# Kernel tuning notes

Measured on AMD Instinct MI355X. Metric: run time of the kernel, lower is better.

## Reference

```python
import jax, jax.numpy as jnp
import numpy as np

V, E, LD, NLANG, H, B, T = 8000, 150, 50, 10, 512, 100, 50
D0 = E + LD  # layer-0 GRU input size


def setup_inputs() -> dict:
    key = jax.random.key(0)
    ks = jax.random.split(key, 12)
    iw = 0.5 / E  # TF init_width
    def rn(k, shape, s=0.05):
        return jax.random.normal(k, shape, jnp.float32) * s
    return {
        "input_data": jax.random.randint(ks[0], (B, T), 0, V, jnp.int32),
        "langs": jax.random.randint(ks[1], (B,), 0, NLANG, jnp.int32),
        "targets": jax.random.randint(ks[2], (B, T), 0, V, jnp.int32),
        "embedding": jax.random.uniform(ks[3], (V, E), jnp.float32, -iw, iw),
        "lang_emb": jax.random.uniform(ks[4], (NLANG, LD), jnp.float32, -iw, iw),
        "Wg0": rn(ks[5], (D0 + H, 2 * H)),
        "bg0": jnp.ones((2 * H,), jnp.float32),  # TF GRUCell bias_start=1.0
        "Wc0": rn(ks[6], (D0 + H, H)),
        "bc0": jnp.zeros((H,), jnp.float32),
        "Wg1": rn(ks[7], (H + H, 2 * H)),
        "bg1": jnp.ones((2 * H,), jnp.float32),
        "Wc1": rn(ks[8], (H + H, H)),
        "bc1": jnp.zeros((H,), jnp.float32),
        "softmax_w": rn(ks[9], (H, V)),
        "softmax_b": jnp.zeros((V,), jnp.float32),
    }


def _l2norm(x):
    return x / jnp.sqrt(jnp.maximum(jnp.sum(x * x, axis=1, keepdims=True), 1e-12))


def _gru(h, x, Wg, bg, Wc, bc):
    # TF GRUCell: r,u = sigmoid([x,h]Wg + bg); c = tanh([x, r*h]Wc + bc)
    ru = jax.nn.sigmoid(jnp.concatenate([x, h], axis=1) @ Wg + bg)
    r, u = jnp.split(ru, 2, axis=1)
    c = jnp.tanh(jnp.concatenate([x, r * h], axis=1) @ Wc + bc)
    return u * h + (1.0 - u) * c


def reference(input_data, langs, targets, embedding, lang_emb,
              Wg0, bg0, Wc0, bc0, Wg1, bg1, Wc1, bc1, softmax_w, softmax_b):
    emb = _l2norm(embedding)[input_data]          # [B,T,E]
    lg = _l2norm(lang_emb)[langs]                 # [B,LD]
    lg = jnp.broadcast_to(lg[:, None, :], (B, T, LD))
    xs = jnp.concatenate([emb, lg], axis=-1)      # [B,T,D0]
    xs = jnp.transpose(xs, (1, 0, 2))             # [T,B,D0]

    def step(carry, x_t):
        h0, h1 = carry
        h0 = _gru(h0, x_t, Wg0, bg0, Wc0, bc0)
        h1 = _gru(h1, h0, Wg1, bg1, Wc1, bc1)
        return (h0, h1), h1

    init = (jnp.zeros((B, H), xs.dtype), jnp.zeros((B, H), xs.dtype))
    _, outs = jax.lax.scan(step, init, xs)        # [T,B,H]
    output = jnp.transpose(outs, (1, 0, 2)).reshape(B * T, H)
    logits = output @ softmax_w + softmax_b       # [B*T,V]
    logp = jax.nn.log_softmax(logits, axis=-1)
    nll = -jnp.take_along_axis(logp, targets.reshape(-1, 1), axis=1)[:, 0]
    cost = jnp.sum(nll) / (B * T)
    return cost
```

## Files before the change

kernel.cpp:

```cpp
#include <hip/hip_runtime.h>
#include <hip/hip_bf16.h>
#include <hip/hip_fp8.h>
#include <math.h>

#define V_    8000
#define E_    150
#define LD_   50
#define H_    512
#define B_    100
#define T_    50
#define D0_   200
#define BT_   5000
#define NV_   8000

typedef __attribute__((ext_vector_type(8))) short short8v;
typedef __attribute__((ext_vector_type(4))) float f32x4;
typedef __attribute__((ext_vector_type(2))) long long2v;

__device__ __forceinline__ float sigmoidf_(float x) { return 1.0f / (1.0f + expf(-x)); }
__device__ __forceinline__ unsigned short f2b(float x) {
    __hip_bfloat16 b = __float2bfloat16(x);
    return *(unsigned short*)&b;
}
__device__ __forceinline__ unsigned char f2e4(float x) {
    __hip_fp8_e4m3 v(x);
    return (unsigned char)v.__x;
}
__device__ __forceinline__ void gload16(const void* g, void* l) {
    __builtin_amdgcn_global_load_lds(
        (__attribute__((address_space(1))) void*)(g),
        (__attribute__((address_space(3))) void*)(l), 16, 0, 0);
}

__global__ __launch_bounds__(256) void norm_rows(const float* __restrict__ in,
                                                 float* __restrict__ out, int R, int C) {
    int row = blockIdx.x;
    if (row >= R) return;
    int tid = threadIdx.x;
    float v = (tid < C) ? in[(size_t)row * C + tid] : 0.f;
    __shared__ float red[256];
    red[tid] = v * v;
    __syncthreads();
    for (int s = 128; s > 0; s >>= 1) {
        if (tid < s) red[tid] += red[tid + s];
        __syncthreads();
    }
    float scale = rsqrtf(fmaxf(red[0], 1e-12f));
    if (tid < C) out[(size_t)row * C + tid] = v * scale;
}

__global__ void build_xs(const int* __restrict__ inp, const int* __restrict__ langs,
                         const float* __restrict__ nemb, const float* __restrict__ nlang,
                         float* __restrict__ xs) {
    int idx = blockIdx.x * 256 + threadIdx.x;
    if (idx >= T_ * B_ * D0_) return;
    int t = idx / (B_ * D0_);
    int rem = idx % (B_ * D0_);
    int b = rem / D0_;
    int e = rem % D0_;
    float v;
    if (e < E_) v = nemb[(size_t)inp[b * T_ + t] * E_ + e];
    else        v = nlang[(size_t)langs[b] * LD_ + (e - E_)];
    xs[idx] = v;
}

__global__ __launch_bounds__(256) void gemm_bias(const float* __restrict__ A,
                                                 const float* __restrict__ Bm,
                                                 const float* __restrict__ bias,
                                                 float* __restrict__ C,
                                                 int M, int N, int K, int ldb) {
    __shared__ __align__(16) float As[16][64];
    __shared__ __align__(16) float Bs[16][64];
    const int tid = threadIdx.x;
    const int tx = tid & 15, ty = tid >> 4;
    const int mBase = blockIdx.y * 64, nBase = blockIdx.x * 64;
    float acc[4][4] = {};
    for (int k0 = 0; k0 < K; k0 += 16) {
        int e = tid * 4;
#pragma unroll
        for (int q = 0; q < 4; ++q) {
            int ee = e + q;
            int r = ee >> 4, kk = ee & 15;
            int gr = mBase + r, gk = k0 + kk;
            As[kk][r] = (gr < M && gk < K) ? A[(size_t)gr * K + gk] : 0.f;
        }
        int bk = tid >> 4, bn = (tid & 15) * 4;
        int gk = k0 + bk;
        float4 bv = make_float4(0.f, 0.f, 0.f, 0.f);
        if (gk < K) bv = *(const float4*)(Bm + (size_t)gk * ldb + nBase + bn);
        *(float4*)&Bs[bk][bn] = bv;
        __syncthreads();
#pragma unroll
        for (int kk = 0; kk < 16; ++kk) {
            const float4 a4 = *(const float4*)&As[kk][ty * 4];
            const float4 b4 = *(const float4*)&Bs[kk][tx * 4];
            float a[4] = {a4.x, a4.y, a4.z, a4.w};
            float b[4] = {b4.x, b4.y, b4.z, b4.w};
#pragma unroll
            for (int i = 0; i < 4; ++i)
#pragma unroll
                for (int j = 0; j < 4; ++j) acc[i][j] += a[i] * b[j];
        }
        __syncthreads();
    }
#pragma unroll
    for (int i = 0; i < 4; ++i) {
        int gr = mBase + ty * 4 + i;
        if (gr < M) {
#pragma unroll
            for (int j = 0; j < 4; ++j) {
                int gc = nBase + tx * 4 + j;
                if (gc < N) C[(size_t)gr * N + gc] = acc[i][j] + bias[gc];
            }
        }
    }
}

__global__ __launch_bounds__(256) void pack_frags(const float* __restrict__ W, int ldw,
                                                  int k0off, int KT, int NT,
                                                  unsigned short* __restrict__ dst) {
    int idx = blockIdx.x * 256 + threadIdx.x;
    if (idx >= KT * NT * 64) return;
    int lane = idx & 63;
    int tile = idx >> 6;
    int nt = tile % NT, kt = tile / NT;
    int n = nt * 16 + (lane & 15);
    int kb = k0off + kt * 32 + (lane >> 4) * 8;
    unsigned short o[8];
#pragma unroll
    for (int j = 0; j < 8; ++j) o[j] = f2b(W[(size_t)(kb + j) * ldw + n]);
    *(uint4*)(dst + (size_t)idx * 8) = *(const uint4*)o;
}

__global__ __launch_bounds__(256) void pack_frags8(const float* __restrict__ W, int ldw,
                                                   int k0off, int KT, int NT,
                                                   unsigned char* __restrict__ dst,
                                                   float scale) {
    int idx = blockIdx.x * 256 + threadIdx.x;
    if (idx >= KT * NT * 64) return;
    int lane = idx & 63;
    int tile = idx >> 6;
    int nt = tile % NT, kt = tile / NT;
    int n = nt * 16 + (lane & 15);
    int kb = k0off + kt * 32 + (lane >> 4) * 8;
    unsigned char o[8];
#pragma unroll
    for (int j = 0; j < 8; ++j) o[j] = f2e4(W[(size_t)(kb + j) * ldw + n] * scale);
    size_t off = ((((size_t)(kt >> 1) * NT + nt) * 64 + lane) << 4) + ((kt & 1) << 3);
    *(unsigned long long*)(dst + off) = *(const unsigned long long*)o;
}

template<int NTW>
__device__ __forceinline__ void mm_phase8s(const unsigned char* gsrc0, int NT,
                                           const unsigned char* a0, unsigned char* wst,
                                           int laneoff, int aoffB, f32x4* acc) {
    const size_t gstride = (size_t)NT * 1024;
#pragma unroll
    for (int nt = 0; nt < NTW; ++nt) gload16(gsrc0 + nt * 1024, wst + nt * 1024);
    __builtin_amdgcn_sched_barrier(0);
#pragma unroll
    for (int nt = 0; nt < NTW; ++nt)
        gload16(gsrc0 + gstride + nt * 1024, wst + (NTW + nt) * 1024);
    __builtin_amdgcn_sched_barrier(0);
#pragma unroll
    for (int ktp = 0; ktp < 8; ++ktp) {
        if (ktp < 7) {
            if (NTW == 4) asm volatile("s_waitcnt vmcnt(4)" ::: "memory");
            else          asm volatile("s_waitcnt vmcnt(2)" ::: "memory");
        } else {
            asm volatile("s_waitcnt vmcnt(0)" ::: "memory");
        }
        __builtin_amdgcn_sched_barrier(0);
        unsigned char* lb = wst + (ktp & 1) * (NTW * 1024);
        long av0 = *(const long*)(a0 + aoffB + (2 * ktp) * 32);
        long av1 = *(const long*)(a0 + aoffB + (2 * ktp + 1) * 32);
#pragma unroll
        for (int nt = 0; nt < NTW; ++nt) {
            long2v bv = *(const long2v*)(lb + nt * 1024 + laneoff);
            acc[nt] = __builtin_amdgcn_mfma_f32_16x16x32_fp8_fp8(av0, bv.x, acc[nt], 0, 0, 0);
            acc[nt] = __builtin_amdgcn_mfma_f32_16x16x32_fp8_fp8(av1, bv.y, acc[nt], 0, 0, 0);
        }
        __builtin_amdgcn_sched_barrier(0);
        if (ktp + 2 < 8) {
#pragma unroll
            for (int nt = 0; nt < NTW; ++nt)
                gload16(gsrc0 + (size_t)(ktp + 2) * gstride + nt * 1024, lb + nt * 1024);
            __builtin_amdgcn_sched_barrier(0);
        }
    }
}

#define INV512_ 0.001953125f
__global__ __launch_bounds__(1024) void rnn_pass8(
    const float* __restrict__ Xg, const float* __restrict__ Xc,
    const unsigned char* __restrict__ Wgf, const unsigned char* __restrict__ Wcf,
    unsigned short* __restrict__ houtb) {
    __shared__ __align__(16) unsigned char hb8[16 * 520];
    __shared__ __align__(16) unsigned char rhb8[16 * 520];
    __shared__ float hf[2 * 512], uf[2 * 512];
    __shared__ __align__(16) unsigned char wstage[16 * 8192];
    const int tid = threadIdx.x;
    const int w = tid >> 6, lane = tid & 63;
    const int arow = lane & 15;
    const int laneoff = lane * 16;
    const int aoffB = arow * 520 + (lane >> 4) * 8;
    const int rb = blockIdx.x * 2;
    unsigned char* wst = wstage + (w << 13);
    const unsigned char* gA = Wgf + ((size_t)(w * 4) * 64) * 16 + laneoff;
    const unsigned char* gB = Wcf + ((size_t)(w * 2) * 64) * 16 + laneoff;

    for (int i = tid; i < 16 * 520; i += 1024) { hb8[i] = 0; rhb8[i] = 0; }
    for (int i = tid; i < 2 * 512; i += 1024) hf[i] = 0.f;
    __syncthreads();

    for (int t = 0; t < T_; ++t) {
        const int m0 = t * 100 + rb, m1 = m0 + 1;
        {
            float xg0v[4], xg1v[4];
            if (lane < 16) {
#pragma unroll
                for (int nt = 0; nt < 4; ++nt) {
                    int col = (w * 4 + nt) * 16 + arow;
                    xg0v[nt] = Xg[(size_t)m0 * 1024 + col];
                    xg1v[nt] = Xg[(size_t)m1 * 1024 + col];
                }
            }
            __builtin_amdgcn_sched_barrier(0);
            f32x4 acc[4];
#pragma unroll
            for (int nt = 0; nt < 4; ++nt) acc[nt] = (f32x4){0.f, 0.f, 0.f, 0.f};
            mm_phase8s<4>(gA, 64, hb8, wst, laneoff, aoffB, acc);
            if (lane < 16) {
#pragma unroll
                for (int nt = 0; nt < 4; ++nt) {
                    int col = (w * 4 + nt) * 16 + arow;
                    float s0 = sigmoidf_(fmaf(acc[nt][0], INV512_, xg0v[nt]));
                    float s1 = sigmoidf_(fmaf(acc[nt][1], INV512_, xg1v[nt]));
                    if (col < 512) {
                        rhb8[col]       = f2e4(16.f * s0 * hf[col]);
                        rhb8[520 + col] = f2e4(16.f * s1 * hf[512 + col]);
                    } else {
                        uf[col - 512] = s0;
                        uf[col]       = s1;
                    }
                }
            }
        }
        __syncthreads();
        {
            float xc0v[2], xc1v[2];
            if (lane < 16) {
#pragma unroll
                for (int nt = 0; nt < 2; ++nt) {
                    int col = (w * 2 + nt) * 16 + arow;
                    xc0v[nt] = Xc[(size_t)m0 * 512 + col];
                    xc1v[nt] = Xc[(size_t)m1 * 512 + col];
                }
            }
            __builtin_amdgcn_sched_barrier(0);
            f32x4 acc[2];
#pragma unroll
            for (int nt = 0; nt < 2; ++nt) acc[nt] = (f32x4){0.f, 0.f, 0.f, 0.f};
            mm_phase8s<2>(gB, 32, rhb8, wst, laneoff, aoffB, acc);
            if (lane < 16) {
#pragma unroll
                for (int nt = 0; nt < 2; ++nt) {
                    int col = (w * 2 + nt) * 16 + arow;
                    float c0 = tanhf(fmaf(acc[nt][0], INV512_, xc0v[nt]));
                    float c1 = tanhf(fmaf(acc[nt][1], INV512_, xc1v[nt]));
                    float uA = uf[col], uB = uf[512 + col];
                    float hA = uA * hf[col] + (1.f - uA) * c0;
                    float hB = uB * hf[512 + col] + (1.f - uB) * c1;
                    hf[col] = hA; hf[512 + col] = hB;
                    hb8[col] = f2e4(16.f * hA); hb8[520 + col] = f2e4(16.f * hB);
                    houtb[(size_t)m0 * 512 + col] = f2b(hA);
                    houtb[(size_t)m1 * 512 + col] = f2b(hB);
                }
            }
        }
        __syncthreads();
    }
}

template<int NTW>
__global__ __launch_bounds__(256) void xproj_mfma(const unsigned short* __restrict__ Abf,
                                                  const unsigned short* __restrict__ Wf,
                                                  const float* __restrict__ bias,
                                                  float* __restrict__ C, int M) {
    const int NT = NTW * 4;
    const int N = NT * 16;
    const int tid = threadIdx.x;
    const int w = tid >> 6, lane = tid & 63;
    const int arow = lane & 15, hi = lane >> 4;
    const int mbase = blockIdx.x * 16;
    int ga = mbase + arow; if (ga >= M) ga = M - 1;
    const unsigned short* ap = Abf + (size_t)ga * 512 + hi * 8;
    f32x4 acc[NTW];
#pragma unroll
    for (int nt = 0; nt < NTW; ++nt) acc[nt] = (f32x4){0.f, 0.f, 0.f, 0.f};
#pragma unroll 2
    for (int kt = 0; kt < 16; ++kt) {
        short8v af = *(const short8v*)(ap + kt * 32);
        const unsigned short* wp = Wf + ((size_t)(kt * NT + w * NTW) * 64 + lane) * 8;
#pragma unroll
        for (int nt = 0; nt < NTW; ++nt) {
            short8v bf = *(const short8v*)(wp + (size_t)nt * 512);
            acc[nt] = __builtin_amdgcn_mfma_f32_16x16x32_bf16(af, bf, acc[nt], 0, 0, 0);
        }
    }
#pragma unroll
    for (int nt = 0; nt < NTW; ++nt) {
        int col = (w * NTW + nt) * 16 + arow;
        float bb = bias[col];
#pragma unroll
        for (int q = 0; q < 4; ++q) {
            int gm = mbase + hi * 4 + q;
            if (gm < M) C[(size_t)gm * N + col] = acc[nt][q] + bb;
        }
    }
}

__global__ __launch_bounds__(256) void lse_mfma(const unsigned short* __restrict__ Abf,
                                                const unsigned short* __restrict__ swf,
                                                const float* __restrict__ sb,
                                                const int* __restrict__ tgt,
                                                float* __restrict__ zt,
                                                float* __restrict__ parts) {
    const int tid = threadIdx.x;
    const int w = tid >> 6, lane = tid & 63;
    const int arow = lane & 15, hi = lane >> 4;
    const int mbase = blockIdx.y * 64 + w * 16;
    const int ntg0 = blockIdx.x * 4;
    int ga = mbase + arow; if (ga >= BT_) ga = BT_ - 1;
    const unsigned short* ap = Abf + (size_t)ga * 512 + hi * 8;
    f32x4 acc[4];
#pragma unroll
    for (int nt = 0; nt < 4; ++nt) acc[nt] = (f32x4){0.f, 0.f, 0.f, 0.f};
#pragma unroll 2
    for (int kt = 0; kt < 16; ++kt) {
        short8v af = *(const short8v*)(ap + kt * 32);
        const unsigned short* wp = swf + ((size_t)(kt * 500 + ntg0) * 64 + lane) * 8;
#pragma unroll
        for (int nt = 0; nt < 4; ++nt) {
            short8v bf = *(const short8v*)(wp + (size_t)nt * 512);
            acc[nt] = __builtin_amdgcn_mfma_f32_16x16x32_bf16(af, bf, acc[nt], 0, 0, 0);
        }
    }
#pragma unroll
    for (int nt = 0; nt < 4; ++nt) {
        float bb = sb[(ntg0 + nt) * 16 + arow];
#pragma unroll
        for (int q = 0; q < 4; ++q) acc[nt][q] += bb;
    }
#pragma unroll
    for (int q = 0; q < 4; ++q) {
        int gr = mbase + hi * 4 + q;
        if (gr < BT_) {
            int tg = tgt[(gr % 100) * 50 + gr / 100];
            int lt = tg - arow;
#pragma unroll
            for (int nt = 0; nt < 4; ++nt)
                if (lt == (ntg0 + nt) * 16) zt[gr] = acc[nt][q];
        }
    }
    float lm[4], ls[4];
#pragma unroll
    for (int q = 0; q < 4; ++q)
        lm[q] = fmaxf(fmaxf(acc[0][q], acc[1][q]), fmaxf(acc[2][q], acc[3][q]));
#pragma unroll
    for (int mask = 1; mask < 16; mask <<= 1)
#pragma unroll
        for (int q = 0; q < 4; ++q) lm[q] = fmaxf(lm[q], __shfl_xor(lm[q], mask));
#pragma unroll
    for (int q = 0; q < 4; ++q) {
        float s = 0.f;
#pragma unroll
        for (int nt = 0; nt < 4; ++nt) s += expf(acc[nt][q] - lm[q]);
        ls[q] = s;
    }
#pragma unroll
    for (int mask = 1; mask < 16; mask <<= 1)
#pragma unroll
        for (int q = 0; q < 4; ++q) ls[q] += __shfl_xor(ls[q], mask);
    if (arow == 0) {
#pragma unroll
        for (int q = 0; q < 4; ++q) {
            int gr = mbase + hi * 4 + q;
            if (gr < BT_) {
                parts[(size_t)gr * 250 + blockIdx.x * 2 + 0] = lm[q];
                parts[(size_t)gr * 250 + blockIdx.x * 2 + 1] = ls[q];
            }
        }
    }
}

__global__ __launch_bounds__(128) void final_nll(const float* __restrict__ parts,
                                                 const float* __restrict__ zt,
                                                 float* __restrict__ bsum) {
    int i = blockIdx.x * 128 + threadIdx.x;
    float nll = 0.f;
    if (i < BT_) {
        const float* p = parts + (size_t)i * 250;
        float M = p[0];
        for (int j = 1; j < 125; ++j) M = fmaxf(M, p[2 * j]);
        float S = 0.f;
        for (int j = 0; j < 125; ++j) S += p[2 * j + 1] * expf(p[2 * j] - M);
        nll = M + logf(S) - zt[i];
    }
    __shared__ float red[128];
    red[threadIdx.x] = nll;
    __syncthreads();
    for (int s = 64; s > 0; s >>= 1) {
        if (threadIdx.x < s) red[threadIdx.x] += red[threadIdx.x + s];
        __syncthreads();
    }
    if (threadIdx.x == 0) bsum[blockIdx.x] = red[0];
}

__global__ __launch_bounds__(64) void final_sum(const float* __restrict__ bsum,
                                                float* __restrict__ out) {
    int tid = threadIdx.x;
    float v = (tid < 40) ? bsum[tid] : 0.f;
    for (int off = 32; off > 0; off >>= 1) v += __shfl_down(v, off);
    if (tid == 0) out[0] = v / 5000.0f;
}

extern "C" void kernel_launch(void* const* d_in, const int* in_sizes, int n_in,
                              void* d_out, int out_size, void* d_ws, size_t ws_size,
                              hipStream_t stream) {
    const int*   inp   = (const int*)d_in[0];
    const int*   langs = (const int*)d_in[1];
    const int*   tgt   = (const int*)d_in[2];
    const float* emb   = (const float*)d_in[3];
    const float* lemb  = (const float*)d_in[4];
    const float* Wg0   = (const float*)d_in[5];
    const float* bg0   = (const float*)d_in[6];
    const float* Wc0   = (const float*)d_in[7];
    const float* bc0   = (const float*)d_in[8];
    const float* Wg1   = (const float*)d_in[9];
    const float* bg1   = (const float*)d_in[10];
    const float* Wc1   = (const float*)d_in[11];
    const float* bc1   = (const float*)d_in[12];
    const float* sw    = (const float*)d_in[13];
    const float* sb    = (const float*)d_in[14];
    float* out = (float*)d_out;

    float* w = (float*)d_ws;
    float* nemb = w;
    unsigned char* a8 = (unsigned char*)w;
    unsigned char* Wg0f8  = a8;
    unsigned char* Wc0f8  = a8 + 524288;
    unsigned char* Wg1hf8 = a8 + 786432;
    unsigned char* Wc1hf8 = a8 + 1310720;
    unsigned short* Wg1xf = (unsigned short*)(a8 + 1572864);
    unsigned short* Wc1xf = Wg1xf + 524288;
    float* nlang = w + 1200000;
    float* xs    = w + 1200512;
    float* Xg0   = w + 2200512;
    float* Xg1   = w + 2200512;
    unsigned short* swf = (unsigned short*)(w + 2200512);
    float* Xc0   = w + 7320512;
    float* Xc1   = w + 7320512;
    float* parts = w + 7320512;
    float* ztb   = w + 7320512 + 1250000;
    float* bsum  = w + 7320512 + 1255000;
    unsigned short* h0seq = (unsigned short*)(w + 9880512);
    unsigned short* h1o   = (unsigned short*)(w + 9880512);

    norm_rows<<<V_, 256, 0, stream>>>(emb, nemb, V_, E_);
    norm_rows<<<10, 256, 0, stream>>>(lemb, nlang, 10, LD_);
    build_xs<<<(T_ * B_ * D0_ + 255) / 256, 256, 0, stream>>>(inp, langs, nemb, nlang, xs);
    pack_frags8<<<256, 256, 0, stream>>>(Wg0, 1024, D0_, 16, 64, Wg0f8, 32.f);
    pack_frags8<<<128, 256, 0, stream>>>(Wc0,  512, D0_, 16, 32, Wc0f8, 32.f);
    pack_frags8<<<256, 256, 0, stream>>>(Wg1, 1024, 512, 16, 64, Wg1hf8, 32.f);
    pack_frags8<<<128, 256, 0, stream>>>(Wc1,  512, 512, 16, 32, Wc1hf8, 32.f);
    pack_frags<<<256, 256, 0, stream>>>(Wg1, 1024, 0, 16, 64, Wg1xf);
    pack_frags<<<128, 256, 0, stream>>>(Wc1,  512, 0, 16, 32, Wc1xf);
    gemm_bias<<<dim3(16, 79), 256, 0, stream>>>(xs, Wg0, bg0, Xg0, BT_, 1024, D0_, 1024);
    gemm_bias<<<dim3(8, 79), 256, 0, stream>>>(xs, Wc0, bc0, Xc0, BT_, 512, D0_, 512);
    rnn_pass8<<<50, 1024, 0, stream>>>(Xg0, Xc0, Wg0f8, Wc0f8, h0seq);
    xproj_mfma<16><<<313, 256, 0, stream>>>(h0seq, Wg1xf, bg1, Xg1, BT_);
    xproj_mfma<8><<<313, 256, 0, stream>>>(h0seq, Wc1xf, bc1, Xc1, BT_);
    rnn_pass8<<<50, 1024, 0, stream>>>(Xg1, Xc1, Wg1hf8, Wc1hf8, h1o);
    pack_frags<<<2000, 256, 0, stream>>>(sw, NV_, 0, 16, 500, swf);
    lse_mfma<<<dim3(125, 79), 256, 0, stream>>>(h1o, swf, sb, tgt, ztb, parts);
    final_nll<<<40, 128, 0, stream>>>(parts, ztb, bsum);
    final_sum<<<1, 64, 0, stream>>>(bsum, out);
}
```

Before: 1.582 ms.

## Use bf16 MFMA for layer-0 input projection and deepen recurrent weight prefetch pipeline

Replaces the scalar fp32 tiled GEMM for the layer-0 input projections with the existing bf16 MFMA xproj kernel. To do this, the inputs are built directly as bf16 with K zero-padded to 224, and the layer-0 weight fragments are packed with a K limit. The recurrent fp8 matmul helper is also restructured into a 3-deep, 4-slot sub-step pipeline of 2 KB chunks with finer vmcnt waits, replacing the double-buffered full-tile loads. The changes target the slow fp32 GEMM and latency stalls in the sequential RNN loop, at the cost of bf16 rounding of the inputs and extra lgkmcnt waits per sub-step.

```diff
diff --git a/kernel.cpp b/kernel.cpp
--- a/kernel.cpp
+++ b/kernel.cpp
@@ -12,6 +12,7 @@
 #define D0_   200
 #define BT_   5000
 #define NV_   8000
+#define KXP_  224
 
 typedef __attribute__((ext_vector_type(8))) short short8v;
 typedef __attribute__((ext_vector_type(4))) float f32x4;
@@ -49,76 +50,22 @@
     if (tid < C) out[(size_t)row * C + tid] = v * scale;
 }
 
-__global__ void build_xs(const int* __restrict__ inp, const int* __restrict__ langs,
-                         const float* __restrict__ nemb, const float* __restrict__ nlang,
-                         float* __restrict__ xs) {
+__global__ void build_xsb(const int* __restrict__ inp, const int* __restrict__ langs,
+                          const float* __restrict__ nemb, const float* __restrict__ nlang,
+                          unsigned short* __restrict__ xsb) {
     int idx = blockIdx.x * 256 + threadIdx.x;
-    if (idx >= T_ * B_ * D0_) return;
-    int t = idx / (B_ * D0_);
-    int rem = idx % (B_ * D0_);
-    int b = rem / D0_;
-    int e = rem % D0_;
-    float v;
-    if (e < E_) v = nemb[(size_t)inp[b * T_ + t] * E_ + e];
-    else        v = nlang[(size_t)langs[b] * LD_ + (e - E_)];
-    xs[idx] = v;
-}
-
-__global__ __launch_bounds__(256) void gemm_bias(const float* __restrict__ A,
-                                                 const float* __restrict__ Bm,
-                                                 const float* __restrict__ bias,
-                                                 float* __restrict__ C,
-                                                 int M, int N, int K, int ldb) {
-    __shared__ __align__(16) float As[16][64];
-    __shared__ __align__(16) float Bs[16][64];
-    const int tid = threadIdx.x;
-    const int tx = tid & 15, ty = tid >> 4;
-    const int mBase = blockIdx.y * 64, nBase = blockIdx.x * 64;
-    float acc[4][4] = {};
-    for (int k0 = 0; k0 < K; k0 += 16) {
-        int e = tid * 4;
-#pragma unroll
-        for (int q = 0; q < 4; ++q) {
-            int ee = e + q;
-            int r = ee >> 4, kk = ee & 15;
-            int gr = mBase + r, gk = k0 + kk;
-            As[kk][r] = (gr < M && gk < K) ? A[(size_t)gr * K + gk] : 0.f;
-        }
-        int bk = tid >> 4, bn = (tid & 15) * 4;
-        int gk = k0 + bk;
-        float4 bv = make_float4(0.f, 0.f, 0.f, 0.f);
-        if (gk < K) bv = *(const float4*)(Bm + (size_t)gk * ldb + nBase + bn);
-        *(float4*)&Bs[bk][bn] = bv;
-        __syncthreads();
-#pragma unroll
-        for (int kk = 0; kk < 16; ++kk) {
-            const float4 a4 = *(const float4*)&As[kk][ty * 4];
-            const float4 b4 = *(const float4*)&Bs[kk][tx * 4];
-            float a[4] = {a4.x, a4.y, a4.z, a4.w};
-            float b[4] = {b4.x, b4.y, b4.z, b4.w};
-#pragma unroll
-            for (int i = 0; i < 4; ++i)
-#pragma unroll
-                for (int j = 0; j < 4; ++j) acc[i][j] += a[i] * b[j];
-        }
-        __syncthreads();
-    }
-#pragma unroll
-    for (int i = 0; i < 4; ++i) {
-        int gr = mBase + ty * 4 + i;
-        if (gr < M) {
-#pragma unroll
-            for (int j = 0; j < 4; ++j) {
-                int gc = nBase + tx * 4 + j;
-                if (gc < N) C[(size_t)gr * N + gc] = acc[i][j] + bias[gc];
-            }
-        }
-    }
+    if (idx >= BT_ * KXP_) return;
+    int m = idx / KXP_, e = idx % KXP_;
+    int b = m % 100, t = m / 100;
+    float v = 0.f;
+    if (e < E_)       v = nemb[(size_t)inp[b * T_ + t] * E_ + e];
+    else if (e < D0_) v = nlang[(size_t)langs[b] * LD_ + (e - E_)];
+    xsb[idx] = f2b(v);
 }
 
 __global__ __launch_bounds__(256) void pack_frags(const float* __restrict__ W, int ldw,
                                                   int k0off, int KT, int NT,
-                                                  unsigned short* __restrict__ dst) {
+                                                  unsigned short* __restrict__ dst, int klim) {
     int idx = blockIdx.x * 256 + threadIdx.x;
     if (idx >= KT * NT * 64) return;
     int lane = idx & 63;
@@ -128,7 +75,8 @@
     int kb = k0off + kt * 32 + (lane >> 4) * 8;
     unsigned short o[8];
 #pragma unroll
-    for (int j = 0; j < 8; ++j) o[j] = f2b(W[(size_t)(kb + j) * ldw + n]);
+    for (int j = 0; j < 8; ++j)
+        o[j] = (kb + j < klim) ? f2b(W[(size_t)(kb + j) * ldw + n]) : 0;
     *(uint4*)(dst + (size_t)idx * 8) = *(const uint4*)o;
 }
 
@@ -150,43 +98,52 @@
     *(unsigned long long*)(dst + off) = *(const unsigned long long*)o;
 }
 
-template<int NTW>
-__device__ __forceinline__ void mm_phase8s(const unsigned char* gsrc0, int NT,
-                                           const unsigned char* a0, unsigned char* wst,
-                                           int laneoff, int aoffB, f32x4* acc) {
+template<int NSUB, int SPK>
+__device__ __forceinline__ void mm_sub(const unsigned char* gsrc0, int NT,
+                                       const unsigned char* a0, unsigned char* wst,
+                                       int laneoff, int aoffB, f32x4* acc) {
     const size_t gstride = (size_t)NT * 1024;
 #pragma unroll
-    for (int nt = 0; nt < NTW; ++nt) gload16(gsrc0 + nt * 1024, wst + nt * 1024);
+    for (int s = 0; s < 3; ++s) {
+        const int ktp = (SPK == 2) ? (s >> 1) : s;
+        const int h = (SPK == 2) ? (s & 1) : 0;
+        const unsigned char* g = gsrc0 + (size_t)ktp * gstride + h * 2048;
+        gload16(g, wst + (s & 3) * 2048);
+        gload16(g + 1024, wst + (s & 3) * 2048 + 1024);
+    }
     __builtin_amdgcn_sched_barrier(0);
 #pragma unroll
-    for (int nt = 0; nt < NTW; ++nt)
-        gload16(gsrc0 + gstride + nt * 1024, wst + (NTW + nt) * 1024);
-    __builtin_amdgcn_sched_barrier(0);
-#pragma unroll
-    for (int ktp = 0; ktp < 8; ++ktp) {
-        if (ktp < 7) {
-            if (NTW == 4) asm volatile("s_waitcnt vmcnt(4)" ::: "memory");
-            else          asm volatile("s_waitcnt vmcnt(2)" ::: "memory");
-        } else {
-            asm volatile("s_waitcnt vmcnt(0)" ::: "memory");
+    for (int s = 0; s < NSUB; ++s) {
+        if (s + 3 < NSUB) {
+            const int s3 = s + 3;
+            const int ktp3 = (SPK == 2) ? (s3 >> 1) : s3;
+            const int h3 = (SPK == 2) ? (s3 & 1) : 0;
+            const unsigned char* g = gsrc0 + (size_t)ktp3 * gstride + h3 * 2048;
+            gload16(g, wst + (s3 & 3) * 2048);
+            gload16(g + 1024, wst + (s3 & 3) * 2048 + 1024);
+            __builtin_amdgcn_sched_barrier(0);
+        }
+        {
+            const int newer = (NSUB - 1 - s) < 3 ? (NSUB - 1 - s) : 3;
+            if (newer == 3)      asm volatile("s_waitcnt vmcnt(6)" ::: "memory");
+            else if (newer == 2) asm volatile("s_waitcnt vmcnt(4)" ::: "memory");
+            else if (newer == 1) asm volatile("s_waitcnt vmcnt(2)" ::: "memory");
+            else                 asm volatile("s_waitcnt vmcnt(0)" ::: "memory");
         }
         __builtin_amdgcn_sched_barrier(0);
-        unsigned char* lb = wst + (ktp & 1) * (NTW * 1024);
+        const int ktp = (SPK == 2) ? (s >> 1) : s;
+        const int h = (SPK == 2) ? (s & 1) : 0;
         long av0 = *(const long*)(a0 + aoffB + (2 * ktp) * 32);
         long av1 = *(const long*)(a0 + aoffB + (2 * ktp + 1) * 32);
-#pragma unroll
-        for (int nt = 0; nt < NTW; ++nt) {
-            long2v bv = *(const long2v*)(lb + nt * 1024 + laneoff);
-            acc[nt] = __builtin_amdgcn_mfma_f32_16x16x32_fp8_fp8(av0, bv.x, acc[nt], 0, 0, 0);
-            acc[nt] = __builtin_amdgcn_mfma_f32_16x16x32_fp8_fp8(av1, bv.y, acc[nt], 0, 0, 0);
-        }
+        const unsigned char* lb = wst + (s & 3) * 2048;
+        long2v bv0 = *(const long2v*)(lb + laneoff);
+        long2v bv1 = *(const long2v*)(lb + 1024 + laneoff);
+        acc[h * 2 + 0] = __builtin_amdgcn_mfma_f32_16x16x32_fp8_fp8(av0, bv0.x, acc[h * 2 + 0], 0, 0, 0);
+        acc[h * 2 + 0] = __builtin_amdgcn_mfma_f32_16x16x32_fp8_fp8(av1, bv0.y, acc[h * 2 + 0], 0, 0, 0);
+        acc[h * 2 + 1] = __builtin_amdgcn_mfma_f32_16x16x32_fp8_fp8(av0, bv1.x, acc[h * 2 + 1], 0, 0, 0);
+        acc[h * 2 + 1] = __builtin_amdgcn_mfma_f32_16x16x32_fp8_fp8(av1, bv1.y, acc[h * 2 + 1], 0, 0, 0);
+        asm volatile("s_waitcnt lgkmcnt(0)" ::: "memory");
         __builtin_amdgcn_sched_barrier(0);
-        if (ktp + 2 < 8) {
-#pragma unroll
-            for (int nt = 0; nt < NTW; ++nt)
-                gload16(gsrc0 + (size_t)(ktp + 2) * gstride + nt * 1024, lb + nt * 1024);
-            __builtin_amdgcn_sched_barrier(0);
-        }
     }
 }
 
@@ -229,7 +186,7 @@
             f32x4 acc[4];
 #pragma unroll
             for (int nt = 0; nt < 4; ++nt) acc[nt] = (f32x4){0.f, 0.f, 0.f, 0.f};
-            mm_phase8s<4>(gA, 64, hb8, wst, laneoff, aoffB, acc);
+            mm_sub<16, 2>(gA, 64, hb8, wst, laneoff, aoffB, acc);
             if (lane < 16) {
 #pragma unroll
                 for (int nt = 0; nt < 4; ++nt) {
@@ -261,7 +218,7 @@
             f32x4 acc[2];
 #pragma unroll
             for (int nt = 0; nt < 2; ++nt) acc[nt] = (f32x4){0.f, 0.f, 0.f, 0.f};
-            mm_phase8s<2>(gB, 32, rhb8, wst, laneoff, aoffB, acc);
+            mm_sub<8, 1>(gB, 32, rhb8, wst, laneoff, aoffB, acc);
             if (lane < 16) {
 #pragma unroll
                 for (int nt = 0; nt < 2; ++nt) {
@@ -282,7 +239,7 @@
     }
 }
 
-template<int NTW>
+template<int NTW, int KT, int LDA>
 __global__ __launch_bounds__(256) void xproj_mfma(const unsigned short* __restrict__ Abf,
                                                   const unsigned short* __restrict__ Wf,
                                                   const float* __restrict__ bias,
@@ -294,12 +251,12 @@
     const int arow = lane & 15, hi = lane >> 4;
     const int mbase = blockIdx.x * 16;
     int ga = mbase + arow; if (ga >= M) ga = M - 1;
-    const unsigned short* ap = Abf + (size_t)ga * 512 + hi * 8;
+    const unsigned short* ap = Abf + (size_t)ga * LDA + hi * 8;
     f32x4 acc[NTW];
 #pragma unroll
     for (int nt = 0; nt < NTW; ++nt) acc[nt] = (f32x4){0.f, 0.f, 0.f, 0.f};
 #pragma unroll 2
-    for (int kt = 0; kt < 16; ++kt) {
+    for (int kt = 0; kt < KT; ++kt) {
         short8v af = *(const short8v*)(ap + kt * 32);
         const unsigned short* wp = Wf + ((size_t)(kt * NT + w * NTW) * 64 + lane) * 8;
 #pragma unroll
@@ -455,7 +412,9 @@
     unsigned short* Wg1xf = (unsigned short*)(a8 + 1572864);
     unsigned short* Wc1xf = Wg1xf + 524288;
     float* nlang = w + 1200000;
-    float* xs    = w + 1200512;
+    unsigned short* xsb   = (unsigned short*)(w + 1200512);
+    unsigned short* Wg0xf = (unsigned short*)(w + 1760512);
+    unsigned short* Wc0xf = (unsigned short*)(w + 1875200);
     float* Xg0   = w + 2200512;
     float* Xg1   = w + 2200512;
     unsigned short* swf = (unsigned short*)(w + 2200512);
@@ -469,20 +428,22 @@
 
     norm_rows<<<V_, 256, 0, stream>>>(emb, nemb, V_, E_);
     norm_rows<<<10, 256, 0, stream>>>(lemb, nlang, 10, LD_);
-    build_xs<<<(T_ * B_ * D0_ + 255) / 256, 256, 0, stream>>>(inp, langs, nemb, nlang, xs);
+    build_xsb<<<(BT_ * KXP_ + 255) / 256, 256, 0, stream>>>(inp, langs, nemb, nlang, xsb);
     pack_frags8<<<256, 256, 0, stream>>>(Wg0, 1024, D0_, 16, 64, Wg0f8, 32.f);
     pack_frags8<<<128, 256, 0, stream>>>(Wc0,  512, D0_, 16, 32, Wc0f8, 32.f);
     pack_frags8<<<256, 256, 0, stream>>>(Wg1, 1024, 512, 16, 64, Wg1hf8, 32.f);
     pack_frags8<<<128, 256, 0, stream>>>(Wc1,  512, 512, 16, 32, Wc1hf8, 32.f);
-    pack_frags<<<256, 256, 0, stream>>>(Wg1, 1024, 0, 16, 64, Wg1xf);
-    pack_frags<<<128, 256, 0, stream>>>(Wc1,  512, 0, 16, 32, Wc1xf);
-    gemm_bias<<<dim3(16, 79), 256, 0, stream>>>(xs, Wg0, bg0, Xg0, BT_, 1024, D0_, 1024);
-    gemm_bias<<<dim3(8, 79), 256, 0, stream>>>(xs, Wc0, bc0, Xc0, BT_, 512, D0_, 512);
+    pack_frags<<<256, 256, 0, stream>>>(Wg1, 1024, 0, 16, 64, Wg1xf, 1 << 30);
+    pack_frags<<<128, 256, 0, stream>>>(Wc1,  512, 0, 16, 32, Wc1xf, 1 << 30);
+    pack_frags<<<112, 256, 0, stream>>>(Wg0, 1024, 0, 7, 64, Wg0xf, D0_);
+    pack_frags<<<56, 256, 0, stream>>>(Wc0,  512, 0, 7, 32, Wc0xf, D0_);
+    xproj_mfma<16, 7, KXP_><<<313, 256, 0, stream>>>(xsb, Wg0xf, bg0, Xg0, BT_);
+    xproj_mfma<8, 7, KXP_><<<313, 256, 0, stream>>>(xsb, Wc0xf, bc0, Xc0, BT_);
     rnn_pass8<<<50, 1024, 0, stream>>>(Xg0, Xc0, Wg0f8, Wc0f8, h0seq);
-    xproj_mfma<16><<<313, 256, 0, stream>>>(h0seq, Wg1xf, bg1, Xg1, BT_);
-    xproj_mfma<8><<<313, 256, 0, stream>>>(h0seq, Wc1xf, bc1, Xc1, BT_);
+    xproj_mfma<16, 16, 512><<<313, 256, 0, stream>>>(h0seq, Wg1xf, bg1, Xg1, BT_);
+    xproj_mfma<8, 16, 512><<<313, 256, 0, stream>>>(h0seq, Wc1xf, bc1, Xc1, BT_);
     rnn_pass8<<<50, 1024, 0, stream>>>(Xg1, Xc1, Wg1hf8, Wc1hf8, h1o);
-    pack_frags<<<2000, 256, 0, stream>>>(sw, NV_, 0, 16, 500, swf);
+    pack_frags<<<2000, 256, 0, stream>>>(sw, NV_, 0, 16, 500, swf, 1 << 30);
     lse_mfma<<<dim3(125, 79), 256, 0, stream>>>(h1o, swf, sb, tgt, ztb, parts);
     final_nll<<<40, 128, 0, stream>>>(parts, ztb, bsum);
     final_sum<<<1, 64, 0, stream>>>(bsum, out);
```

Result: slower. 1.676 ms (+5.9%).
